# Kernel tuning notes

Hardware: AMD Instinct MI355X
Metric: run time of the kernel (lower is better)

## Reference

```python
import jax, jax.numpy as jnp
import numpy as np

B = 131072          # batch size
D = 128             # input_dim
OUT = 64            # output_dim
L = 32              # number of masked (CustomizedLinear) layers = hidden + output nodes


def setup_inputs() -> dict:
    key = jax.random.key(0)
    ks = jax.random.split(key, 8)
    x = jax.random.normal(ks[0], (B, D), dtype=jnp.float32)
    # start_node: nn.Linear(D, D)
    w_start = jax.random.normal(ks[1], (D, D), dtype=jnp.float32) / np.sqrt(D)
    b_start = jnp.zeros((D,), dtype=jnp.float32)
    # masked linear layers: weight elementwise-multiplied by binary graph mask
    raw_w = jax.random.normal(ks[2], (L, D, D), dtype=jnp.float32) / np.sqrt(D)
    mask = (jax.random.uniform(ks[3], (L, D, D)) < 0.25).astype(jnp.float32)
    masked_w = raw_w * mask          # [L, D, D]
    layer_b = jnp.zeros((L, D), dtype=jnp.float32)
    # output_layer: nn.Linear(D, OUT)
    w_out = jax.random.normal(ks[4], (OUT, D), dtype=jnp.float32) / np.sqrt(D)
    b_out = jnp.zeros((OUT,), dtype=jnp.float32)
    return {"x": x, "w_start": w_start, "b_start": b_start,
            "masked_w": masked_w, "layer_b": layer_b,
            "w_out": w_out, "b_out": b_out}


def reference(x, w_start, b_start, masked_w, layer_b, w_out, b_out):
    # x = start_node(x)
    x0 = x @ w_start.T + b_start          # [B, D]

    # sequential masked-linear chain with relu + residual back to x0
    def step(h, params):
        w, b = params                      # w: [D, D], b: [D]
        h = jax.nn.relu(h @ w.T + b) + x0  # x_ = relu(layer(x_)) + x
        return h, None

    h, _ = jax.lax.scan(step, x0, (masked_w, layer_b))

    logits = h @ w_out.T + b_out          # [B, OUT]
    return jax.nn.softmax(logits, axis=1)
```

## Files before the change

kernel.cpp:

```cpp
#include <hip/hip_runtime.h>
#include <hip/hip_bf16.h>
#include <stdint.h>


typedef short bs8 __attribute__((ext_vector_type(8)));
typedef float f32x4 __attribute__((ext_vector_type(4)));

union Frag { bs8 v; uint32_t u[4]; };
union F4   { float4 f; f32x4 v; };

__device__ __forceinline__ uint32_t cvtpk(float lo, float hi) {
#if __has_builtin(__builtin_amdgcn_cvt_pk_bf16_f32)
  auto r = __builtin_amdgcn_cvt_pk_bf16_f32(lo, hi);
  uint32_t u; __builtin_memcpy(&u, &r, 4);
  return u;
#else
  union { float f; uint32_t u; } a, b; a.f = lo; b.f = hi;
  uint32_t ra = a.u + 0x7fffu + ((a.u >> 16) & 1u);
  uint32_t rb = b.u + 0x7fffu + ((b.u >> 16) & 1u);
  return (ra >> 16) | (rb & 0xffff0000u);
#endif
}

__global__ void prep_frags(const float* __restrict__ w_start,
                           const float* __restrict__ masked_w,
                           const float* __restrict__ w_out,
                           uint16_t* __restrict__ dst) {
  int t = blockIdx.x * 256 + threadIdx.x;
  if (t >= 68608) return;
  int lane = t & 63, kt = (t >> 6) & 3, q = lane >> 4, m15 = lane & 15;
  float f[8];
  if (t < 2048) {
    int nt = (t >> 8) & 7;
    const float* s = w_start + (nt * 16 + m15) * 128 + q * 8 + kt * 32;
    #pragma unroll
    for (int j = 0; j < 8; ++j) f[j] = s[j];
  } else if (t < 67584) {
    int t2 = t - 2048, l = t2 >> 11, nt = (t2 >> 8) & 7;
    const float* s = masked_w + ((l * 128) + nt * 16 + m15) * 128 + q * 4 + kt * 32;
    #pragma unroll
    for (int j = 0; j < 8; ++j) f[j] = s[(j & 3) + 16 * (j >> 2)];
  } else {
    int t3 = t - 67584, nt = (t3 >> 8) & 3;
    const float* s = w_out + (nt * 16 + m15) * 128 + q * 4 + kt * 32;
    #pragma unroll
    for (int j = 0; j < 8; ++j) f[j] = s[(j & 3) + 16 * (j >> 2)];
  }
  uint4 o;
  o.x = cvtpk(f[0], f[1]); o.y = cvtpk(f[2], f[3]);
  o.z = cvtpk(f[4], f[5]); o.w = cvtpk(f[6], f[7]);
  *reinterpret_cast<uint4*>(dst + t * 8) = o;
}

extern __shared__ uint16_t lds[];

__global__ void __launch_bounds__(256, 3)
wann_main(const float* __restrict__ x,
          const float* __restrict__ b_start,
          const float* __restrict__ layer_b,
          const float* __restrict__ b_out,
          const uint16_t* __restrict__ wfrag,
          float* __restrict__ out) {
  const int tid  = threadIdx.x;
  const int lane = tid & 63;
  const int wave = tid >> 6;
  const int q    = lane >> 4;
  const int mc   = lane & 15;
  const long batch0 = (long)blockIdx.x * 128 + wave * 32;
  const f32x4 zero4 = {0.f, 0.f, 0.f, 0.f};

  uint16_t* X = lds;
  uint16_t* Y = lds + 8192;

  auto stage = [&](uint16_t* dstb, const uint16_t* srcb) {
    #pragma unroll
    for (int i = 0; i < 4; ++i) {
      __builtin_amdgcn_global_load_lds(
          (const __attribute__((address_space(1))) void*)(srcb + i * 2048 + wave * 512 + lane * 8),
          (__attribute__((address_space(3))) void*)(dstb + i * 2048 + wave * 512),
          16, 0, 0);
    }
  };

  stage(X, wfrag);

  Frag xf[2][4];
  #pragma unroll
  for (int mt = 0; mt < 2; ++mt) {
    const float* xrow = x + (batch0 + mt * 16 + mc) * 128 + q * 8;
    #pragma unroll
    for (int kt = 0; kt < 4; ++kt) {
      float4 a = *reinterpret_cast<const float4*>(xrow + kt * 32);
      float4 b = *reinterpret_cast<const float4*>(xrow + kt * 32 + 4);
      xf[mt][kt].u[0] = cvtpk(a.x, a.y);
      xf[mt][kt].u[1] = cvtpk(a.z, a.w);
      xf[mt][kt].u[2] = cvtpk(b.x, b.y);
      xf[mt][kt].u[3] = cvtpk(b.z, b.w);
    }
  }

  Frag x0f[2][4], hA[2][4], hB[2][4];

  auto start_half = [&](const uint16_t* buf, int p0, const F4* bb) {
    #pragma unroll
    for (int pp = 0; pp < 2; ++pp) {
      const int p = p0 + pp;
      f32x4 acc[2][2];
      #pragma unroll
      for (int kt = 0; kt < 4; ++kt)
        #pragma unroll
        for (int ntl = 0; ntl < 2; ++ntl) {
          const int ntloc = 2 * pp + ntl;
          Frag wf;
          wf.v = *reinterpret_cast<const bs8*>(buf + ((ntloc * 4 + kt) * 64 + lane) * 8);
          #pragma unroll
          for (int mt = 0; mt < 2; ++mt) {
            f32x4 c = (kt == 0) ? bb[2 * p + ntl].v : acc[ntl][mt];
            acc[ntl][mt] = __builtin_amdgcn_mfma_f32_16x16x32_bf16(wf.v, xf[mt][kt].v, c, 0, 0, 0);
          }
        }
      #pragma unroll
      for (int mt = 0; mt < 2; ++mt)
        #pragma unroll
        for (int ntl = 0; ntl < 2; ++ntl) {
          x0f[mt][p].u[2 * ntl + 0] = cvtpk(acc[ntl][mt][0], acc[ntl][mt][1]);
          x0f[mt][p].u[2 * ntl + 1] = cvtpk(acc[ntl][mt][2], acc[ntl][mt][3]);
        }
    }
  };

  auto chain_half = [&](const uint16_t* buf, int p0, const F4* bb,
                        Frag (&hin)[2][4], Frag (&hout)[2][4]) {
    #pragma unroll
    for (int pp = 0; pp < 2; ++pp) {
      const int p = p0 + pp;
      f32x4 acc[2][2];
      #pragma unroll
      for (int kt = 0; kt < 4; ++kt)
        #pragma unroll
        for (int ntl = 0; ntl < 2; ++ntl) {
          const int ntloc = 2 * pp + ntl;
          Frag wf;
          wf.v = *reinterpret_cast<const bs8*>(buf + ((ntloc * 4 + kt) * 64 + lane) * 8);
          #pragma unroll
          for (int mt = 0; mt < 2; ++mt) {
            f32x4 c = (kt == 0) ? bb[2 * p + ntl].v : acc[ntl][mt];
            acc[ntl][mt] = __builtin_amdgcn_mfma_f32_16x16x32_bf16(wf.v, hin[mt][kt].v, c, 0, 0, 0);
          }
        }
      #pragma unroll
      for (int mt = 0; mt < 2; ++mt)
        #pragma unroll
        for (int ntl = 0; ntl < 2; ++ntl) {
          f32x4 r = __builtin_elementwise_max(acc[ntl][mt], zero4);
          uint32_t xw0 = x0f[mt][p].u[2 * ntl + 0];
          uint32_t xw1 = x0f[mt][p].u[2 * ntl + 1];
          f32x4 xv;
          xv[0] = __uint_as_float(xw0 << 16);
          xv[1] = __uint_as_float(xw0 & 0xffff0000u);
          xv[2] = __uint_as_float(xw1 << 16);
          xv[3] = __uint_as_float(xw1 & 0xffff0000u);
          r = r + xv;
          hout[mt][p].u[2 * ntl + 0] = cvtpk(r[0], r[1]);
          hout[mt][p].u[2 * ntl + 1] = cvtpk(r[2], r[3]);
        }
    }
  };

  F4 barr[8];
  #pragma unroll
  for (int nt = 0; nt < 8; ++nt)
    barr[nt].f = *reinterpret_cast<const float4*>(b_start + nt * 16 + q * 4);

  __syncthreads();
  stage(Y, wfrag + 8192);
  start_half(X, 0, barr);
  __syncthreads();
  const uint16_t* chain = wfrag + 16384;
  stage(X, chain);
  start_half(Y, 2, barr);
  #pragma unroll
  for (int mt = 0; mt < 2; ++mt)
    #pragma unroll
    for (int kt = 0; kt < 4; ++kt)
      hA[mt][kt].v = x0f[mt][kt].v;

  #pragma unroll 1
  for (int l = 0; l < 32; l += 2) {
    __syncthreads();
    stage(Y, chain + l * 16384 + 8192);
    {
      const float* bl = layer_b + l * 128;
      #pragma unroll
      for (int nt = 0; nt < 8; ++nt)
        barr[nt].f = *reinterpret_cast<const float4*>(bl + nt * 16 + q * 4);
    }
    chain_half(X, 0, barr, hA, hB);
    __syncthreads();
    stage(X, chain + (l + 1) * 16384);
    chain_half(Y, 2, barr, hA, hB);

    __syncthreads();
    stage(Y, chain + (l + 1) * 16384 + 8192);
    {
      const float* bl = layer_b + (l + 1) * 128;
      #pragma unroll
      for (int nt = 0; nt < 8; ++nt)
        barr[nt].f = *reinterpret_cast<const float4*>(bl + nt * 16 + q * 4);
    }
    chain_half(X, 0, barr, hB, hA);
    __syncthreads();
    if (l + 2 < 32) stage(X, chain + (l + 2) * 16384);
    chain_half(Y, 2, barr, hB, hA);
  }
  __syncthreads();

  const uint16_t* wout = wfrag + 540672;
  F4 bo[4];
  #pragma unroll
  for (int nt = 0; nt < 4; ++nt)
    bo[nt].f = *reinterpret_cast<const float4*>(b_out + nt * 16 + q * 4);
  f32x4 ao[4][2];
  #pragma unroll
  for (int kt = 0; kt < 4; ++kt) {
    #pragma unroll
    for (int nt = 0; nt < 4; ++nt) {
      Frag wf;
      wf.v = *reinterpret_cast<const bs8*>(wout + ((nt * 4 + kt) * 64 + lane) * 8);
      #pragma unroll
      for (int mt = 0; mt < 2; ++mt) {
        f32x4 c = (kt == 0) ? bo[nt].v : ao[nt][mt];
        ao[nt][mt] = __builtin_amdgcn_mfma_f32_16x16x32_bf16(wf.v, hA[mt][kt].v, c, 0, 0, 0);
      }
    }
  }

  float* tr = reinterpret_cast<float*>(lds) + wave * 1088;
  #pragma unroll
  for (int mt = 0; mt < 2; ++mt) {
    float e[16];
    float M = -3.0e38f;
    #pragma unroll
    for (int nt = 0; nt < 4; ++nt)
      #pragma unroll
      for (int r = 0; r < 4; ++r)
        M = fmaxf(M, ao[nt][mt][r]);
    M = fmaxf(M, __shfl_xor(M, 16, 64));
    M = fmaxf(M, __shfl_xor(M, 32, 64));
    float S = 0.0f;
    #pragma unroll
    for (int nt = 0; nt < 4; ++nt)
      #pragma unroll
      for (int r = 0; r < 4; ++r) {
        float t = exp2f((ao[nt][mt][r] - M) * 1.4426950408889634f);
        e[nt * 4 + r] = t;
        S += t;
      }
    S += __shfl_xor(S, 16, 64);
    S += __shfl_xor(S, 32, 64);
    const float inv = 1.0f / S;
    #pragma unroll
    for (int nt = 0; nt < 4; ++nt) {
      float4 pv;
      pv.x = e[nt * 4 + 0] * inv;
      pv.y = e[nt * 4 + 1] * inv;
      pv.z = e[nt * 4 + 2] * inv;
      pv.w = e[nt * 4 + 3] * inv;
      *reinterpret_cast<float4*>(tr + mc * 68 + nt * 16 + q * 4) = pv;
    }
    __asm__ volatile("s_waitcnt lgkmcnt(0)" ::: "memory");
    #pragma unroll
    for (int it = 0; it < 4; ++it) {
      int row = it * 4 + (lane >> 4);
      float4 v = *reinterpret_cast<const float4*>(tr + row * 68 + (lane & 15) * 4);
      long gr = batch0 + mt * 16 + row;
      *reinterpret_cast<float4*>(out + gr * 64 + (lane & 15) * 4) = v;
    }
    __asm__ volatile("s_waitcnt lgkmcnt(0)" ::: "memory");
  }
}

extern "C" void kernel_launch(void* const* d_in, const int* in_sizes, int n_in,
                              void* d_out, int out_size, void* d_ws, size_t ws_size,
                              hipStream_t stream) {
  const float* x        = (const float*)d_in[0];
  const float* w_start  = (const float*)d_in[1];
  const float* b_start  = (const float*)d_in[2];
  const float* masked_w = (const float*)d_in[3];
  const float* layer_b  = (const float*)d_in[4];
  const float* w_out    = (const float*)d_in[5];
  const float* b_out    = (const float*)d_in[6];
  uint16_t* wfrag = (uint16_t*)d_ws;

  prep_frags<<<268, 256, 0, stream>>>(w_start, masked_w, w_out, wfrag);
  wann_main<<<1024, 256, 32768, stream>>>(x, b_start, layer_b, b_out, wfrag,
                                          (float*)d_out);
}
```

Measured before the change: 286.3 us.

## Triple-buffer weight chunks in LDS with biases packed and vmcnt-based barriers

Repacks the weight fragments into 67 chunks of 8320 halfwords, each carrying its bias vector, so a single async global->LDS stage brings in both weights and bias. The main kernel moves from a double buffer to a three-slot ring, prefetching two chunks ahead. It replaces __syncthreads with an explicit vmcnt wait plus a raw s_barrier, and wraps the MFMA loops in s_setprio. The goal is to hide weight-load latency and remove the per-layer global bias loads. The cost is LDS growing to about 49 KB, which may limit blocks per CU, and the hand-counted vmcnt waits are fragile.

```diff
diff --git a/kernel.cpp b/kernel.cpp
--- a/kernel.cpp
+++ b/kernel.cpp
@@ -23,25 +23,43 @@
 }
 
 __global__ void prep_frags(const float* __restrict__ w_start,
+                           const float* __restrict__ b_start,
                            const float* __restrict__ masked_w,
+                           const float* __restrict__ layer_b,
                            const float* __restrict__ w_out,
+                           const float* __restrict__ b_out,
                            uint16_t* __restrict__ dst) {
   int t = blockIdx.x * 256 + threadIdx.x;
-  if (t >= 68608) return;
+  if (t >= 69680) return;
+  if (t >= 68608) {
+    int f = (t - 68608) * 4;
+    int c, off; const float* src;
+    if (f < 128)       { c = f >> 6;               off = f & 63; src = b_start + f; }
+    else if (f < 4224) { int g = f - 128;  c = 2 + (g >> 6); off = g & 63; src = layer_b + g; }
+    else               { int g = f - 4224; c = 66;           off = g;      src = b_out + g; }
+    float4 v = *reinterpret_cast<const float4*>(src);
+    *reinterpret_cast<float4*>(
+        reinterpret_cast<float*>(dst + (size_t)c * 8320 + 8192) + off) = v;
+    return;
+  }
   int lane = t & 63, kt = (t >> 6) & 3, q = lane >> 4, m15 = lane & 15;
   float f[8];
+  int c, ntloc;
   if (t < 2048) {
     int nt = (t >> 8) & 7;
+    c = nt >> 2; ntloc = nt & 3;
     const float* s = w_start + (nt * 16 + m15) * 128 + q * 8 + kt * 32;
     #pragma unroll
     for (int j = 0; j < 8; ++j) f[j] = s[j];
   } else if (t < 67584) {
     int t2 = t - 2048, l = t2 >> 11, nt = (t2 >> 8) & 7;
+    c = 2 + 2 * l + (nt >> 2); ntloc = nt & 3;
     const float* s = masked_w + ((l * 128) + nt * 16 + m15) * 128 + q * 4 + kt * 32;
     #pragma unroll
     for (int j = 0; j < 8; ++j) f[j] = s[(j & 3) + 16 * (j >> 2)];
   } else {
     int t3 = t - 67584, nt = (t3 >> 8) & 3;
+    c = 66; ntloc = nt;
     const float* s = w_out + (nt * 16 + m15) * 128 + q * 4 + kt * 32;
     #pragma unroll
     for (int j = 0; j < 8; ++j) f[j] = s[(j & 3) + 16 * (j >> 2)];
@@ -49,16 +67,16 @@
   uint4 o;
   o.x = cvtpk(f[0], f[1]); o.y = cvtpk(f[2], f[3]);
   o.z = cvtpk(f[4], f[5]); o.w = cvtpk(f[6], f[7]);
-  *reinterpret_cast<uint4*>(dst + t * 8) = o;
+  *reinterpret_cast<uint4*>(dst + (size_t)c * 8320 +
+                            ((ntloc * 4 + kt) * 64 + lane) * 8) = o;
 }
 
 extern __shared__ uint16_t lds[];
+
+#define VMW(N) asm volatile("s_waitcnt vmcnt(" #N ")" ::: "memory")
 
 __global__ void __launch_bounds__(256, 3)
 wann_main(const float* __restrict__ x,
-          const float* __restrict__ b_start,
-          const float* __restrict__ layer_b,
-          const float* __restrict__ b_out,
           const uint16_t* __restrict__ wfrag,
           float* __restrict__ out) {
   const int tid  = threadIdx.x;
@@ -69,10 +87,10 @@
   const long batch0 = (long)blockIdx.x * 128 + wave * 32;
   const f32x4 zero4 = {0.f, 0.f, 0.f, 0.f};
 
-  uint16_t* X = lds;
-  uint16_t* Y = lds + 8192;
-
-  auto stage = [&](uint16_t* dstb, const uint16_t* srcb) {
+  auto slotp = [&](uint32_t s) -> uint16_t* { return lds + (size_t)s * 8320; };
+
+  auto stage = [&](uint16_t* dstb, uint32_t c) {
+    const uint16_t* srcb = wfrag + (size_t)c * 8320;
     #pragma unroll
     for (int i = 0; i < 4; ++i) {
       __builtin_amdgcn_global_load_lds(
@@ -80,9 +98,17 @@
           (__attribute__((address_space(3))) void*)(dstb + i * 2048 + wave * 512),
           16, 0, 0);
     }
+    __builtin_amdgcn_global_load_lds(
+        (const __attribute__((address_space(1))) void*)(srcb + 8192 + lane * 2),
+        (__attribute__((address_space(3))) void*)(dstb + 8192),
+        4, 0, 0);
   };
 
-  stage(X, wfrag);
+  auto barx = [&]() {
+    asm volatile("" ::: "memory");
+    __builtin_amdgcn_s_barrier();
+    asm volatile("" ::: "memory");
+  };
 
   Frag xf[2][4];
   #pragma unroll
@@ -99,13 +125,22 @@
     }
   }
 
+  stage(slotp(0), 0);
+  stage(slotp(1), 1);
+
   Frag x0f[2][4], hA[2][4], hB[2][4];
 
-  auto start_half = [&](const uint16_t* buf, int p0, const F4* bb) {
+  auto start_half = [&](const uint16_t* buf, int h) {
+    const float* bbb = reinterpret_cast<const float*>(buf + 8192);
     #pragma unroll
     for (int pp = 0; pp < 2; ++pp) {
-      const int p = p0 + pp;
+      const int p = 2 * h + pp;
+      F4 bb[2];
+      #pragma unroll
+      for (int ntl = 0; ntl < 2; ++ntl)
+        bb[ntl].f = *reinterpret_cast<const float4*>(bbb + (2 * pp + ntl) * 16 + q * 4);
       f32x4 acc[2][2];
+      __builtin_amdgcn_s_setprio(1);
       #pragma unroll
       for (int kt = 0; kt < 4; ++kt)
         #pragma unroll
@@ -115,10 +150,11 @@
           wf.v = *reinterpret_cast<const bs8*>(buf + ((ntloc * 4 + kt) * 64 + lane) * 8);
           #pragma unroll
           for (int mt = 0; mt < 2; ++mt) {
-            f32x4 c = (kt == 0) ? bb[2 * p + ntl].v : acc[ntl][mt];
+            f32x4 c = (kt == 0) ? bb[ntl].v : acc[ntl][mt];
             acc[ntl][mt] = __builtin_amdgcn_mfma_f32_16x16x32_bf16(wf.v, xf[mt][kt].v, c, 0, 0, 0);
           }
         }
+      __builtin_amdgcn_s_setprio(0);
       #pragma unroll
       for (int mt = 0; mt < 2; ++mt)
         #pragma unroll
@@ -129,12 +165,18 @@
     }
   };
 
-  auto chain_half = [&](const uint16_t* buf, int p0, const F4* bb,
+  auto chain_half = [&](const uint16_t* buf, int h,
                         Frag (&hin)[2][4], Frag (&hout)[2][4]) {
+    const float* bbb = reinterpret_cast<const float*>(buf + 8192);
     #pragma unroll
     for (int pp = 0; pp < 2; ++pp) {
-      const int p = p0 + pp;
+      const int p = 2 * h + pp;
+      F4 bb[2];
+      #pragma unroll
+      for (int ntl = 0; ntl < 2; ++ntl)
+        bb[ntl].f = *reinterpret_cast<const float4*>(bbb + (2 * pp + ntl) * 16 + q * 4);
       f32x4 acc[2][2];
+      __builtin_amdgcn_s_setprio(1);
       #pragma unroll
       for (int kt = 0; kt < 4; ++kt)
         #pragma unroll
@@ -144,10 +186,11 @@
           wf.v = *reinterpret_cast<const bs8*>(buf + ((ntloc * 4 + kt) * 64 + lane) * 8);
           #pragma unroll
           for (int mt = 0; mt < 2; ++mt) {
-            f32x4 c = (kt == 0) ? bb[2 * p + ntl].v : acc[ntl][mt];
+            f32x4 c = (kt == 0) ? bb[ntl].v : acc[ntl][mt];
             acc[ntl][mt] = __builtin_amdgcn_mfma_f32_16x16x32_bf16(wf.v, hin[mt][kt].v, c, 0, 0, 0);
           }
         }
+      __builtin_amdgcn_s_setprio(0);
       #pragma unroll
       for (int mt = 0; mt < 2; ++mt)
         #pragma unroll
@@ -167,66 +210,50 @@
     }
   };
 
-  F4 barr[8];
-  #pragma unroll
-  for (int nt = 0; nt < 8; ++nt)
-    barr[nt].f = *reinterpret_cast<const float4*>(b_start + nt * 16 + q * 4);
-
-  __syncthreads();
-  stage(Y, wfrag + 8192);
-  start_half(X, 0, barr);
-  __syncthreads();
-  const uint16_t* chain = wfrag + 16384;
-  stage(X, chain);
-  start_half(Y, 2, barr);
+  VMW(5); barx(); stage(slotp(2), 2);
+  start_half(slotp(0), 0);
+  VMW(5); barx(); stage(slotp(0), 3);
+  start_half(slotp(1), 1);
   #pragma unroll
   for (int mt = 0; mt < 2; ++mt)
     #pragma unroll
     for (int kt = 0; kt < 4; ++kt)
       hA[mt][kt].v = x0f[mt][kt].v;
 
+  uint32_t s0 = 2;
   #pragma unroll 1
   for (int l = 0; l < 32; l += 2) {
-    __syncthreads();
-    stage(Y, chain + l * 16384 + 8192);
-    {
-      const float* bl = layer_b + l * 128;
-      #pragma unroll
-      for (int nt = 0; nt < 8; ++nt)
-        barr[nt].f = *reinterpret_cast<const float4*>(bl + nt * 16 + q * 4);
-    }
-    chain_half(X, 0, barr, hA, hB);
-    __syncthreads();
-    stage(X, chain + (l + 1) * 16384);
-    chain_half(Y, 2, barr, hA, hB);
-
-    __syncthreads();
-    stage(Y, chain + (l + 1) * 16384 + 8192);
-    {
-      const float* bl = layer_b + (l + 1) * 128;
-      #pragma unroll
-      for (int nt = 0; nt < 8; ++nt)
-        barr[nt].f = *reinterpret_cast<const float4*>(bl + nt * 16 + q * 4);
-    }
-    chain_half(X, 0, barr, hB, hA);
-    __syncthreads();
-    if (l + 2 < 32) stage(X, chain + (l + 2) * 16384);
-    chain_half(Y, 2, barr, hB, hA);
-  }
-  __syncthreads();
-
-  const uint16_t* wout = wfrag + 540672;
+    const uint32_t s1 = (s0 + 1 < 3) ? s0 + 1 : 0;
+    const uint32_t s2 = (s1 + 1 < 3) ? s1 + 1 : 0;
+    const uint32_t c0 = 2 + 2 * (uint32_t)l;
+
+    VMW(5); barx(); stage(slotp(s2), c0 + 2);
+    chain_half(slotp(s0), 0, hA, hB);
+    VMW(5); barx(); stage(slotp(s0), c0 + 3);
+    chain_half(slotp(s1), 1, hA, hB);
+    VMW(5); barx(); if (c0 + 4 <= 66) stage(slotp(s1), c0 + 4);
+    chain_half(slotp(s2), 0, hB, hA);
+    VMW(5); barx(); if (c0 + 5 <= 66) stage(slotp(s2), c0 + 5);
+    chain_half(slotp(s0), 1, hB, hA);
+
+    s0 = s1;
+  }
+
+  VMW(0); barx();
+  const uint16_t* wo = slotp(0);
+  const float* bob = reinterpret_cast<const float*>(wo + 8192);
   F4 bo[4];
   #pragma unroll
   for (int nt = 0; nt < 4; ++nt)
-    bo[nt].f = *reinterpret_cast<const float4*>(b_out + nt * 16 + q * 4);
+    bo[nt].f = *reinterpret_cast<const float4*>(bob + nt * 16 + q * 4);
   f32x4 ao[4][2];
+  __builtin_amdgcn_s_setprio(1);
   #pragma unroll
   for (int kt = 0; kt < 4; ++kt) {
     #pragma unroll
     for (int nt = 0; nt < 4; ++nt) {
       Frag wf;
-      wf.v = *reinterpret_cast<const bs8*>(wout + ((nt * 4 + kt) * 64 + lane) * 8);
+      wf.v = *reinterpret_cast<const bs8*>(wo + ((nt * 4 + kt) * 64 + lane) * 8);
       #pragma unroll
       for (int mt = 0; mt < 2; ++mt) {
         f32x4 c = (kt == 0) ? bo[nt].v : ao[nt][mt];
@@ -234,8 +261,10 @@
       }
     }
   }
-
-  float* tr = reinterpret_cast<float*>(lds) + wave * 1088;
+  __builtin_amdgcn_s_setprio(0);
+
+  float* tr = reinterpret_cast<float*>(reinterpret_cast<char*>(lds) + 16640)
+              + wave * 1088;
   #pragma unroll
   for (int mt = 0; mt < 2; ++mt) {
     float e[16];
@@ -292,7 +321,7 @@
   const float* b_out    = (const float*)d_in[6];
   uint16_t* wfrag = (uint16_t*)d_ws;
 
-  prep_frags<<<268, 256, 0, stream>>>(w_start, masked_w, w_out, wfrag);
-  wann_main<<<1024, 256, 32768, stream>>>(x, b_start, layer_b, b_out, wfrag,
-                                          (float*)d_out);
+  prep_frags<<<273, 256, 0, stream>>>(w_start, b_start, masked_w, layer_b,
+                                      w_out, b_out, wfrag);
+  wann_main<<<1024, 256, 49920, stream>>>(x, wfrag, (float*)d_out);
 }
```

Measured after the change: 270.2 us. 1.06x faster.
